# Kernel optimization log

Measured on AMD Instinct MI355X. Metric: run time of the kernel, lower is better.

Reference implementation:

```python
import jax, jax.numpy as jnp
import numpy as np

B, S, DIM, HEADS, MLP = 2, 2048, 1024, 16, 4096
DH = DIM // HEADS
LN_EPS = 1e-5


def layernorm(x, g, b):
    m = x.mean(-1, keepdims=True)
    v = ((x - m) ** 2).mean(-1, keepdims=True)
    return (x - m) / jnp.sqrt(v + LN_EPS) * g + b


def rope(x):
    # x: [B, H, S, dh]; interleaved-pair RoPE (rotary_embedding_torch convention)
    dh = x.shape[-1]
    s = x.shape[-2]
    inv_freq = 1.0 / (10000.0 ** (jnp.arange(0, dh, 2, dtype=jnp.float32) / dh))
    freqs = jnp.arange(s, dtype=jnp.float32)[:, None] * inv_freq[None, :]  # [S, dh/2]
    cos = jnp.repeat(jnp.cos(freqs), 2, axis=-1)  # [S, dh]
    sin = jnp.repeat(jnp.sin(freqs), 2, axis=-1)
    xp = x.reshape(x.shape[:-1] + (dh // 2, 2))
    x_rot = jnp.stack([-xp[..., 1], xp[..., 0]], axis=-1).reshape(x.shape)
    return x * cos + x_rot * sin


def setup_inputs() -> dict:
    key = jax.random.key(0)
    ks = jax.random.split(key, 10)
    w = 0.02
    return {
        "x": jax.random.normal(ks[0], (B, S, DIM), jnp.float32),
        "bias": jax.random.normal(ks[1], (B, S, S), jnp.float32) * 0.1,
        "ln1_g": jnp.ones((DIM,), jnp.float32),
        "ln1_b": jnp.zeros((DIM,), jnp.float32),
        "W_qkv": jax.random.normal(ks[2], (DIM, 3 * DIM), jnp.float32) * w,
        "W_o": jax.random.normal(ks[3], (DIM, DIM), jnp.float32) * w,
        "ln2_g": jnp.ones((DIM,), jnp.float32),
        "ln2_b": jnp.zeros((DIM,), jnp.float32),
        "W1": jax.random.normal(ks[4], (DIM, MLP), jnp.float32) * w,
        "b1": jnp.zeros((MLP,), jnp.float32),
        "W2": jax.random.normal(ks[5], (MLP, DIM), jnp.float32) * w,
        "b2": jnp.zeros((DIM,), jnp.float32),
        "pad_mask": jnp.zeros((B, S), jnp.int32),
    }


def reference(x, bias, ln1_g, ln1_b, W_qkv, W_o, ln2_g, ln2_b, W1, b1, W2, b2, pad_mask):
    b, s, d = x.shape
    h, dh = HEADS, DH
    res = x
    x1 = layernorm(x, ln1_g, ln1_b)
    qkv = (x1 @ W_qkv).reshape(b, s, h, 3 * dh)
    q, k, v = jnp.split(qkv, 3, axis=-1)            # each [B,S,H,dh]
    q = rope(q.transpose(0, 2, 1, 3))               # [B,H,S,dh]
    k = rope(k.transpose(0, 2, 1, 3))
    v = v.transpose(0, 2, 1, 3)
    scores = jnp.einsum("bhqd,bhkd->bhqk", q, k) * (dh ** -0.5)
    scores = scores + bias[:, None]                 # additive bias per batch
    key_mask = pad_mask.astype(bool)[:, None, None, :]
    scores = jnp.where(key_mask, -jnp.inf, scores)
    attn = jax.nn.softmax(scores, axis=-1)          # dropout = identity (eval)
    out = jnp.einsum("bhqk,bhkd->bhqd", attn, v)
    out = out.transpose(0, 2, 1, 3).reshape(b, s, d)
    x = res + out @ W_o
    res2 = x
    x2 = layernorm(x, ln2_g, ln2_b)
    mlp = jax.nn.gelu(x2 @ W1 + b1, approximate=False) @ W2 + b2
    return res2 + mlp
```

## Files before the change

### kernel.cpp

```cpp
#include <hip/hip_runtime.h>
#include <hip/hip_bf16.h>

#define B_   2
#define S_   2048
#define DIM_ 1024
#define H_   16
#define DH_  64
#define MLP_ 4096

typedef __bf16 bf16x8 __attribute__((ext_vector_type(8)));
typedef float  f32x4  __attribute__((ext_vector_type(4)));

__device__ __forceinline__ ushort f2bf(float f) {
    union { float f; unsigned u; } x; x.f = f;
    unsigned r = x.u + 0x7FFFu + ((x.u >> 16) & 1u);
    return (ushort)(r >> 16);
}
__device__ __forceinline__ float bf2f(ushort b) {
    union { unsigned u; float f; } x; x.u = ((unsigned)b) << 16;
    return x.f;
}

#define GLOAD_LDS16(gptr, lptr)                                                        \
    __builtin_amdgcn_global_load_lds(                                                  \
        (const __attribute__((address_space(1))) unsigned int*)(const void*)(gptr),    \
        (__attribute__((address_space(3))) unsigned int*)(void*)(lptr), 16, 0, 0)

#define MFMA_BF16(a, b, c) __builtin_amdgcn_mfma_f32_16x16x32_bf16((a), (b), (c), 0, 0, 0)

__global__ __launch_bounds__(256) void transpose_all(const float* __restrict__ Wqkv, ushort* __restrict__ Wqkvt,
                                                     const float* __restrict__ Wo,   ushort* __restrict__ Wot,
                                                     const float* __restrict__ W1,   ushort* __restrict__ W1t,
                                                     const float* __restrict__ W2,   ushort* __restrict__ W2t) {
    int id = blockIdx.x;
    const float* in; ushort* outp; int K, N, nx;
    if (id < 3072)      { in = Wqkv; outp = Wqkvt; K = 1024; N = 3072; nx = 96;  }
    else if (id < 4096) { id -= 3072; in = Wo; outp = Wot;  K = 1024; N = 1024; nx = 32;  }
    else if (id < 8192) { id -= 4096; in = W1; outp = W1t;  K = 1024; N = 4096; nx = 128; }
    else                { id -= 8192; in = W2; outp = W2t;  K = 4096; N = 1024; nx = 32;  }
    int n0 = (id % nx) * 32, k0 = (id / nx) * 32;
    __shared__ float t[32][33];
    int tx = threadIdx.x, ty = threadIdx.y;
#pragma unroll
    for (int r = 0; r < 32; r += 8)
        t[ty + r][tx] = in[(size_t)(k0 + ty + r) * N + n0 + tx];
    __syncthreads();
#pragma unroll
    for (int r = 0; r < 32; r += 8)
        outp[(size_t)(n0 + ty + r) * K + k0 + tx] = f2bf(t[tx][ty + r]);
}

__global__ __launch_bounds__(256) void ln_kernel(const float* __restrict__ in,
                                                 const float* __restrict__ g,
                                                 const float* __restrict__ beta,
                                                 ushort* __restrict__ out) {
    int row = blockIdx.x;
    float4 v = reinterpret_cast<const float4*>(in + (size_t)row * DIM_)[threadIdx.x];
    float s = v.x + v.y + v.z + v.w;
    float s2 = v.x * v.x + v.y * v.y + v.z * v.z + v.w * v.w;
#pragma unroll
    for (int m = 1; m < 64; m <<= 1) { s += __shfl_xor(s, m); s2 += __shfl_xor(s2, m); }
    __shared__ float red[8];
    int wid = threadIdx.x >> 6;
    if ((threadIdx.x & 63) == 0) { red[wid] = s; red[4 + wid] = s2; }
    __syncthreads();
    s  = red[0] + red[1] + red[2] + red[3];
    s2 = red[4] + red[5] + red[6] + red[7];
    float mean = s * (1.f / DIM_);
    float var  = s2 * (1.f / DIM_) - mean * mean;
    float inv  = rsqrtf(var + 1e-5f);
    float4 gg = reinterpret_cast<const float4*>(g)[threadIdx.x];
    float4 bb = reinterpret_cast<const float4*>(beta)[threadIdx.x];
    ushort4 o;
    o.x = f2bf((v.x - mean) * inv * gg.x + bb.x);
    o.y = f2bf((v.y - mean) * inv * gg.y + bb.y);
    o.z = f2bf((v.z - mean) * inv * gg.z + bb.z);
    o.w = f2bf((v.w - mean) * inv * gg.w + bb.w);
    reinterpret_cast<ushort4*>(out + (size_t)row * DIM_)[threadIdx.x] = o;
}

template <int RM, int RN, bool BIAS, bool GELU, bool RES, bool OBF16>
__global__ __launch_bounds__(256) void gemm_bt(const ushort* __restrict__ A,
                                               const ushort* __restrict__ Bt,
                                               void* __restrict__ Cout,
                                               const float* __restrict__ bias,
                                               const float* __restrict__ resid,
                                               int M, int N, int K) {
    constexpr int BM = RM * 64, BN = RN * 64;
    __shared__ __align__(16) ushort As[2][BM * 32];
    __shared__ __align__(16) ushort Bs[2][BN * 32];
    int tid = threadIdx.x;
    int wid = tid >> 6, lane = tid & 63;
    int lr = lane & 15, lg = lane >> 4;

    int nbx = gridDim.x;
    int nwg = nbx * gridDim.y;
    int bid = blockIdx.y * nbx + blockIdx.x;
    int swz = (bid & 7) * (nwg >> 3) + (bid >> 3);
    int row0 = (swz / nbx) * BM, col0 = (swz % nbx) * BN;

    int wm = (wid >> 1) * (RM * 32), wn = (wid & 1) * (RN * 32);
    int srow = tid >> 2, scol = (tid & 3) * 8;

    f32x4 acc[RM * 2][RN * 2] = {};

    const ushort* gA = A + (size_t)(row0 + srow) * K + scol;
    const ushort* gB = Bt + (size_t)(col0 + srow) * K + scol;

    auto stage = [&](int buf, int kt) {
#pragma unroll
        for (int r = 0; r < RM; r++)
            GLOAD_LDS16(gA + (size_t)r * 64 * K + kt, As[buf] + r * 2048 + wid * 512);
#pragma unroll
        for (int r = 0; r < RN; r++)
            GLOAD_LDS16(gB + (size_t)r * 64 * K + kt, Bs[buf] + r * 2048 + wid * 512);
    };

    int nk = K >> 5;
    stage(0, 0);
    __syncthreads();

    for (int t = 0; t < nk; t++) {
        int cur = t & 1;
        if (t + 1 < nk) stage(cur ^ 1, (t + 1) << 5);
        bf16x8 af[RM * 2], bfr[RN * 2];
#pragma unroll
        for (int m = 0; m < RM * 2; m++)
            af[m] = *reinterpret_cast<const bf16x8*>(As[cur] + (wm + m * 16 + lr) * 32 + lg * 8);
#pragma unroll
        for (int n = 0; n < RN * 2; n++)
            bfr[n] = *reinterpret_cast<const bf16x8*>(Bs[cur] + (wn + n * 16 + lr) * 32 + lg * 8);
#pragma unroll
        for (int m = 0; m < RM * 2; m++)
#pragma unroll
            for (int n = 0; n < RN * 2; n++)
                acc[m][n] = MFMA_BF16(af[m], bfr[n], acc[m][n]);
        __syncthreads();
    }

#pragma unroll
    for (int m = 0; m < RM * 2; m++) {
#pragma unroll
        for (int n = 0; n < RN * 2; n++) {
            int col = col0 + wn + n * 16 + lr;
#pragma unroll
            for (int i = 0; i < 4; i++) {
                int row = row0 + wm + m * 16 + lg * 4 + i;
                float v = acc[m][n][i];
                if (BIAS) v += bias[col];
                if (GELU) v = 0.5f * v * (1.f + erff(v * 0.70710678118f));
                if (RES)  v += resid[(size_t)row * N + col];
                if (OBF16) ((ushort*)Cout)[(size_t)row * N + col] = f2bf(v);
                else       ((float*)Cout)[(size_t)row * N + col] = v;
            }
        }
    }
}

__global__ __launch_bounds__(256) void gemm_qkv(const ushort* __restrict__ A,
                                                const ushort* __restrict__ Bt,
                                                const float2* __restrict__ tab,
                                                ushort* __restrict__ Qr,
                                                ushort* __restrict__ Kr,
                                                ushort* __restrict__ VT) {
    const int K = DIM_, N = 3 * DIM_;
    __shared__ __align__(16) ushort As[2][128 * 32];
    __shared__ __align__(16) ushort Bs[2][128 * 32];
    int tid = threadIdx.x;
    int wid = tid >> 6, lane = tid & 63;
    int lr = lane & 15, lg = lane >> 4;

    int nbx = gridDim.x;
    int nwg = nbx * gridDim.y;
    int bid = blockIdx.y * nbx + blockIdx.x;
    int swz = (bid & 7) * (nwg >> 3) + (bid >> 3);
    int row0 = (swz / nbx) * 128, col0 = (swz % nbx) * 128;

    int wm = (wid >> 1) * 64, wn = (wid & 1) * 64;
    int srow = tid >> 2, scol = (tid & 3) * 8;

    f32x4 acc[4][4] = {};

    const ushort* gA = A + (size_t)(row0 + srow) * K + scol;
    const ushort* gB = Bt + (size_t)(col0 + srow) * K + scol;

    auto stage = [&](int buf, int kt) {
#pragma unroll
        for (int r = 0; r < 2; r++)
            GLOAD_LDS16(gA + (size_t)r * 64 * K + kt, As[buf] + r * 2048 + wid * 512);
#pragma unroll
        for (int r = 0; r < 2; r++)
            GLOAD_LDS16(gB + (size_t)r * 64 * K + kt, Bs[buf] + r * 2048 + wid * 512);
    };

    int nk = K >> 5;
    stage(0, 0);
    __syncthreads();

    for (int t = 0; t < nk; t++) {
        int cur = t & 1;
        if (t + 1 < nk) stage(cur ^ 1, (t + 1) << 5);
        bf16x8 af[4], bfr[4];
#pragma unroll
        for (int m = 0; m < 4; m++)
            af[m] = *reinterpret_cast<const bf16x8*>(As[cur] + (wm + m * 16 + lr) * 32 + lg * 8);
#pragma unroll
        for (int n = 0; n < 4; n++)
            bfr[n] = *reinterpret_cast<const bf16x8*>(Bs[cur] + (wn + n * 16 + lr) * 32 + lg * 8);
#pragma unroll
        for (int m = 0; m < 4; m++)
#pragma unroll
            for (int n = 0; n < 4; n++)
                acc[m][n] = MFMA_BF16(af[m], bfr[n], acc[m][n]);
        __syncthreads();
    }

#pragma unroll
    for (int n = 0; n < 4; n++) {
        int colb = col0 + wn + n * 16;
        int h    = colb / 192;
        int off  = colb % 192;
        int typ  = off >> 6;
        int d    = (off & 63) + lr;
#pragma unroll
        for (int m = 0; m < 4; m++) {
            if (typ < 2) {
                ushort* qk = (typ == 0) ? Qr : Kr;
#pragma unroll
                for (int i = 0; i < 4; i++) {
                    int row = row0 + wm + m * 16 + lg * 4 + i;
                    int b = row >> 11, s = row & (S_ - 1);
                    float v  = acc[m][n][i];
                    float pv = __shfl_xor(v, 1);
                    float2 cs = tab[(s << 5) + (d >> 1)];
                    float r = v * cs.x + ((d & 1) ? pv : -pv) * cs.y;
                    qk[((size_t)(b * H_ + h) * S_ + s) * DH_ + d] = f2bf(r);
                }
            } else {
                int row = row0 + wm + m * 16 + lg * 4;
                int b = row >> 11, s = row & (S_ - 1);
                ushort4 o4;
                o4.x = f2bf(acc[m][n][0]);
                o4.y = f2bf(acc[m][n][1]);
                o4.z = f2bf(acc[m][n][2]);
                o4.w = f2bf(acc[m][n][3]);
                *reinterpret_cast<ushort4*>(
                    VT + ((size_t)(b * H_ + h) * DH_ + d) * S_ + s) = o4;
            }
        }
    }
}

__global__ __launch_bounds__(256) void rope_table(float2* __restrict__ tab) {
    int i = blockIdx.x * 256 + threadIdx.x;
    int s = i >> 5, p = i & 31;
    float invf = __expf(-((float)(2 * p) / 64.f) * logf(10000.f));
    float a = (float)s * invf;
    tab[i] = make_float2(cosf(a), sinf(a));
}

__global__ __launch_bounds__(256) void attn_kernel(const ushort* __restrict__ Q,
                                                   const ushort* __restrict__ Kr,
                                                   const ushort* __restrict__ VT,
                                                   const float* __restrict__ bias,
                                                   const int* __restrict__ pad,
                                                   ushort* __restrict__ Out) {
    int bx = blockIdx.x;
    int qt = bx & 31, h = (bx >> 5) & 15, b = bx >> 9;
    __shared__ __align__(16) ushort Ks[64 * 72];
    __shared__ __align__(16) ushort Vs[64 * 72];
    __shared__ __align__(16) ushort Ps[64 * 72];
    int tid = threadIdx.x, wid = tid >> 6, lane = tid & 63;
    int lr = lane & 15, lg = lane >> 4;
    int q0 = qt * 64;
    const ushort* Qb = Q + ((size_t)(b * H_ + h) * S_) * DH_;
    const ushort* Kb = Kr + ((size_t)(b * H_ + h) * S_) * DH_;
    const ushort* Vb = VT + ((size_t)(b * H_ + h) * DH_) * S_;
    const float*  bb = bias + (size_t)b * S_ * S_;
    const int*    pb = pad + b * S_;

    bf16x8 qf[2];
#pragma unroll
    for (int ks = 0; ks < 2; ks++)
        qf[ks] = *reinterpret_cast<const bf16x8*>(
            Qb + (size_t)(q0 + wid * 16 + lr) * DH_ + ks * 32 + lg * 8);

    float mrow[4], lrow[4];
#pragma unroll
    for (int i = 0; i < 4; i++) { mrow[i] = -3e38f; lrow[i] = 0.f; }
    f32x4 o[4] = {};

    int sr = tid >> 3, sc = (tid & 7) * 8;
    const float scale = 0.125f;

    for (int kv0 = 0; kv0 < S_; kv0 += 64) {
        __syncthreads();
#pragma unroll
        for (int cc = 0; cc < 2; cc++) {
            int r = cc * 32 + sr;
            *reinterpret_cast<bf16x8*>(Ks + r * 72 + sc) =
                *reinterpret_cast<const bf16x8*>(Kb + (size_t)(kv0 + r) * DH_ + sc);
            *reinterpret_cast<bf16x8*>(Vs + r * 72 + sc) =
                *reinterpret_cast<const bf16x8*>(Vb + (size_t)r * S_ + kv0 + sc);
        }
        __syncthreads();

        f32x4 sa[4] = {};
#pragma unroll
        for (int n = 0; n < 4; n++) {
            bf16x8 k0 = *reinterpret_cast<const bf16x8*>(Ks + (n * 16 + lr) * 72 + lg * 8);
            bf16x8 k1 = *reinterpret_cast<const bf16x8*>(Ks + (n * 16 + lr) * 72 + 32 + lg * 8);
            sa[n] = MFMA_BF16(qf[0], k0, sa[n]);
            sa[n] = MFMA_BF16(qf[1], k1, sa[n]);
        }

        int pm[4];
#pragma unroll
        for (int n = 0; n < 4; n++) pm[n] = pb[kv0 + n * 16 + lr];

#pragma unroll
        for (int i = 0; i < 4; i++) {
            const float* brow = bb + (size_t)(q0 + wid * 16 + lg * 4 + i) * S_ + kv0;
            float sv[4];
            float rmax = -3e38f;
#pragma unroll
            for (int n = 0; n < 4; n++) {
                float s = sa[n][i] * scale + brow[n * 16 + lr];
                if (pm[n]) s = -1e30f;
                sv[n] = s;
                rmax = fmaxf(rmax, s);
            }
#pragma unroll
            for (int msk = 1; msk < 16; msk <<= 1) rmax = fmaxf(rmax, __shfl_xor(rmax, msk));
            float mnew = fmaxf(mrow[i], rmax);
            float resc = __expf(mrow[i] - mnew);
            mrow[i] = mnew;
            float ls = 0.f;
            int prow = (i << 2) | lg;
#pragma unroll
            for (int n = 0; n < 4; n++) {
                float p = __expf(sv[n] - mnew);
                ls += p;
                Ps[(wid * 16 + prow) * 72 + n * 16 + lr] = f2bf(p);
            }
            lrow[i] = lrow[i] * resc + ls;
#pragma unroll
            for (int fn = 0; fn < 4; fn++) o[fn][i] *= resc;
        }

        int plr = ((lr & 3) << 2) | (lr >> 2);
        bf16x8 pf0 = *reinterpret_cast<const bf16x8*>(Ps + (wid * 16 + plr) * 72 + lg * 8);
        bf16x8 pf1 = *reinterpret_cast<const bf16x8*>(Ps + (wid * 16 + plr) * 72 + 32 + lg * 8);

#pragma unroll
        for (int fn = 0; fn < 4; fn++) {
            bf16x8 v0 = *reinterpret_cast<const bf16x8*>(Vs + (fn * 16 + lr) * 72 + lg * 8);
            bf16x8 v1 = *reinterpret_cast<const bf16x8*>(Vs + (fn * 16 + lr) * 72 + 32 + lg * 8);
            o[fn] = MFMA_BF16(pf0, v0, o[fn]);
            o[fn] = MFMA_BF16(pf1, v1, o[fn]);
        }
    }

#pragma unroll
    for (int i = 0; i < 4; i++)
#pragma unroll
        for (int msk = 1; msk < 16; msk <<= 1) lrow[i] += __shfl_xor(lrow[i], msk);

#pragma unroll
    for (int fn = 0; fn < 4; fn++)
#pragma unroll
        for (int i = 0; i < 4; i++) {
            int qrow = q0 + wid * 16 + lg * 4 + i;
            Out[(size_t)(b * S_ + qrow) * DIM_ + h * DH_ + fn * 16 + lr] =
                f2bf(o[fn][i] / lrow[i]);
        }
}

extern "C" void kernel_launch(void* const* d_in, const int* in_sizes, int n_in,
                              void* d_out, int out_size, void* d_ws, size_t ws_size,
                              hipStream_t stream) {
    const float* x    = (const float*)d_in[0];
    const float* bias = (const float*)d_in[1];
    const float* ln1g = (const float*)d_in[2];
    const float* ln1b = (const float*)d_in[3];
    const float* Wqkv = (const float*)d_in[4];
    const float* Wo   = (const float*)d_in[5];
    const float* ln2g = (const float*)d_in[6];
    const float* ln2b = (const float*)d_in[7];
    const float* W1   = (const float*)d_in[8];
    const float* b1   = (const float*)d_in[9];
    const float* W2   = (const float*)d_in[10];
    const float* b2   = (const float*)d_in[11];
    const int*   pad  = (const int*)d_in[12];
    float* out = (float*)d_out;

    char* ws = (char*)d_ws;
    size_t off = 0;
    auto alloc = [&](size_t bytes) {
        char* p = ws + off;
        off += (bytes + 255) & ~(size_t)255;
        return (void*)p;
    };
    ushort* x1    = (ushort*)alloc((size_t)4096 * 1024 * 2);
    ushort* Wqkvt = (ushort*)alloc((size_t)3072 * 1024 * 2);
    float2* tab   = (float2*)alloc((size_t)S_ * 32 * 8);
    ushort* Qr    = (ushort*)alloc((size_t)B_ * H_ * S_ * DH_ * 2);
    ushort* Kr2   = (ushort*)alloc((size_t)B_ * H_ * S_ * DH_ * 2);
    ushort* attnO = (ushort*)alloc((size_t)4096 * 1024 * 2);
    ushort* Wot   = (ushort*)alloc((size_t)1024 * 1024 * 2);
    float*  xmid  = (float*)alloc((size_t)4096 * 1024 * 4);
    ushort* x2    = (ushort*)alloc((size_t)4096 * 1024 * 2);
    ushort* W1t   = (ushort*)alloc((size_t)4096 * 1024 * 2);
    ushort* h1    = (ushort*)alloc((size_t)4096 * 4096 * 2);
    ushort* W2t   = (ushort*)alloc((size_t)1024 * 4096 * 2);
    ushort* VT    = h1;

    dim3 tb(32, 8);
    transpose_all<<<12288, tb, 0, stream>>>(Wqkv, Wqkvt, Wo, Wot, W1, W1t, W2, W2t);

    rope_table<<<(S_ * 32) / 256, 256, 0, stream>>>(tab);

    ln_kernel<<<4096, 256, 0, stream>>>(x, ln1g, ln1b, x1);

    gemm_qkv<<<dim3(24, 32), 256, 0, stream>>>(x1, Wqkvt, tab, Qr, Kr2, VT);

    attn_kernel<<<B_ * H_ * (S_ / 64), 256, 0, stream>>>(Qr, Kr2, VT, bias, pad, attnO);

    gemm_bt<1, 2, false, false, true, false><<<dim3(8, 64), 256, 0, stream>>>(
        attnO, Wot, xmid, nullptr, x, 4096, 1024, 1024);

    ln_kernel<<<4096, 256, 0, stream>>>(xmid, ln2g, ln2b, x2);

    gemm_bt<2, 2, true, true, false, true><<<dim3(32, 32), 256, 0, stream>>>(
        x2, W1t, h1, b1, nullptr, 4096, 4096, 1024);

    gemm_bt<1, 2, true, false, true, false><<<dim3(8, 64), 256, 0, stream>>>(
        h1, W2t, out, b2, xmid, 4096, 1024, 4096);
}
```

Measured before the change: 332.5 us.

## Use 512-thread 128x256 tiles for QKV and W1 GEMMs; use native bf16 convert

Adds 512-thread GEMM variants with a 128x256 output tile, eight waves each owning a 64x64 sub-tile, and switches the QKV projection and the first MLP GEMM to them. The wider tile increases A-tile reuse and halves the workgroup count, cutting global loads per FLOP. The cost is more LDS per block and fewer blocks to fill the CUs. The float-to-bf16 helper now uses the compiler's native conversion instead of manual rounding bit tricks.

Result: faster. 314.8 us (median of 2 runs) (-5.3%).

```diff
diff --git a/kernel.cpp b/kernel.cpp
--- a/kernel.cpp
+++ b/kernel.cpp
@@ -12,9 +12,8 @@
 typedef float  f32x4  __attribute__((ext_vector_type(4)));
 
 __device__ __forceinline__ ushort f2bf(float f) {
-    union { float f; unsigned u; } x; x.f = f;
-    unsigned r = x.u + 0x7FFFu + ((x.u >> 16) & 1u);
-    return (ushort)(r >> 16);
+    __bf16 h = (__bf16)f;
+    return __builtin_bit_cast(ushort, h);
 }
 __device__ __forceinline__ float bf2f(ushort b) {
     union { unsigned u; float f; } x; x.u = ((unsigned)b) << 16;
@@ -157,15 +156,15 @@
     }
 }
 
-__global__ __launch_bounds__(256) void gemm_qkv(const ushort* __restrict__ A,
-                                                const ushort* __restrict__ Bt,
-                                                const float2* __restrict__ tab,
-                                                ushort* __restrict__ Qr,
-                                                ushort* __restrict__ Kr,
-                                                ushort* __restrict__ VT) {
-    const int K = DIM_, N = 3 * DIM_;
+template <bool BIAS, bool GELU, bool RES, bool OBF16>
+__global__ __launch_bounds__(512) void gemm_bt512(const ushort* __restrict__ A,
+                                                  const ushort* __restrict__ Bt,
+                                                  void* __restrict__ Cout,
+                                                  const float* __restrict__ bias,
+                                                  const float* __restrict__ resid,
+                                                  int M, int N, int K) {
     __shared__ __align__(16) ushort As[2][128 * 32];
-    __shared__ __align__(16) ushort Bs[2][128 * 32];
+    __shared__ __align__(16) ushort Bs[2][256 * 32];
     int tid = threadIdx.x;
     int wid = tid >> 6, lane = tid & 63;
     int lr = lane & 15, lg = lane >> 4;
@@ -174,9 +173,9 @@
     int nwg = nbx * gridDim.y;
     int bid = blockIdx.y * nbx + blockIdx.x;
     int swz = (bid & 7) * (nwg >> 3) + (bid >> 3);
-    int row0 = (swz / nbx) * 128, col0 = (swz % nbx) * 128;
-
-    int wm = (wid >> 1) * 64, wn = (wid & 1) * 64;
+    int row0 = (swz / nbx) * 128, col0 = (swz % nbx) * 256;
+
+    int wm = (wid >> 2) * 64, wn = (wid & 3) * 64;
     int srow = tid >> 2, scol = (tid & 3) * 8;
 
     f32x4 acc[4][4] = {};
@@ -185,12 +184,83 @@
     const ushort* gB = Bt + (size_t)(col0 + srow) * K + scol;
 
     auto stage = [&](int buf, int kt) {
-#pragma unroll
-        for (int r = 0; r < 2; r++)
-            GLOAD_LDS16(gA + (size_t)r * 64 * K + kt, As[buf] + r * 2048 + wid * 512);
-#pragma unroll
-        for (int r = 0; r < 2; r++)
-            GLOAD_LDS16(gB + (size_t)r * 64 * K + kt, Bs[buf] + r * 2048 + wid * 512);
+        GLOAD_LDS16(gA + kt, As[buf] + wid * 512);
+        GLOAD_LDS16(gB + kt, Bs[buf] + wid * 512);
+        GLOAD_LDS16(gB + (size_t)128 * K + kt, Bs[buf] + 4096 + wid * 512);
+    };
+
+    int nk = K >> 5;
+    stage(0, 0);
+    __syncthreads();
+
+    for (int t = 0; t < nk; t++) {
+        int cur = t & 1;
+        if (t + 1 < nk) stage(cur ^ 1, (t + 1) << 5);
+        bf16x8 af[4], bfr[4];
+#pragma unroll
+        for (int m = 0; m < 4; m++)
+            af[m] = *reinterpret_cast<const bf16x8*>(As[cur] + (wm + m * 16 + lr) * 32 + lg * 8);
+#pragma unroll
+        for (int n = 0; n < 4; n++)
+            bfr[n] = *reinterpret_cast<const bf16x8*>(Bs[cur] + (wn + n * 16 + lr) * 32 + lg * 8);
+#pragma unroll
+        for (int m = 0; m < 4; m++)
+#pragma unroll
+            for (int n = 0; n < 4; n++)
+                acc[m][n] = MFMA_BF16(af[m], bfr[n], acc[m][n]);
+        __syncthreads();
+    }
+
+#pragma unroll
+    for (int m = 0; m < 4; m++) {
+#pragma unroll
+        for (int n = 0; n < 4; n++) {
+            int col = col0 + wn + n * 16 + lr;
+#pragma unroll
+            for (int i = 0; i < 4; i++) {
+                int row = row0 + wm + m * 16 + lg * 4 + i;
+                float v = acc[m][n][i];
+                if (BIAS) v += bias[col];
+                if (GELU) v = 0.5f * v * (1.f + erff(v * 0.70710678118f));
+                if (RES)  v += resid[(size_t)row * N + col];
+                if (OBF16) ((ushort*)Cout)[(size_t)row * N + col] = f2bf(v);
+                else       ((float*)Cout)[(size_t)row * N + col] = v;
+            }
+        }
+    }
+}
+
+__global__ __launch_bounds__(512) void gemm_qkv512(const ushort* __restrict__ A,
+                                                   const ushort* __restrict__ Bt,
+                                                   const float2* __restrict__ tab,
+                                                   ushort* __restrict__ Qr,
+                                                   ushort* __restrict__ Kr,
+                                                   ushort* __restrict__ VT) {
+    const int K = DIM_;
+    __shared__ __align__(16) ushort As[2][128 * 32];
+    __shared__ __align__(16) ushort Bs[2][256 * 32];
+    int tid = threadIdx.x;
+    int wid = tid >> 6, lane = tid & 63;
+    int lr = lane & 15, lg = lane >> 4;
+
+    int nbx = gridDim.x;
+    int nwg = nbx * gridDim.y;
+    int bid = blockIdx.y * nbx + blockIdx.x;
+    int swz = (bid & 7) * (nwg >> 3) + (bid >> 3);
+    int row0 = (swz / nbx) * 128, col0 = (swz % nbx) * 256;
+
+    int wm = (wid >> 2) * 64, wn = (wid & 3) * 64;
+    int srow = tid >> 2, scol = (tid & 3) * 8;
+
+    f32x4 acc[4][4] = {};
+
+    const ushort* gA = A + (size_t)(row0 + srow) * K + scol;
+    const ushort* gB = Bt + (size_t)(col0 + srow) * K + scol;
+
+    auto stage = [&](int buf, int kt) {
+        GLOAD_LDS16(gA + kt, As[buf] + wid * 512);
+        GLOAD_LDS16(gB + kt, Bs[buf] + wid * 512);
+        GLOAD_LDS16(gB + (size_t)128 * K + kt, Bs[buf] + 4096 + wid * 512);
     };
 
     int nk = K >> 5;
@@ -422,7 +492,7 @@
 
     ln_kernel<<<4096, 256, 0, stream>>>(x, ln1g, ln1b, x1);
 
-    gemm_qkv<<<dim3(24, 32), 256, 0, stream>>>(x1, Wqkvt, tab, Qr, Kr2, VT);
+    gemm_qkv512<<<dim3(12, 32), 512, 0, stream>>>(x1, Wqkvt, tab, Qr, Kr2, VT);
 
     attn_kernel<<<B_ * H_ * (S_ / 64), 256, 0, stream>>>(Qr, Kr2, VT, bias, pad, attnO);
 
@@ -431,7 +501,7 @@
 
     ln_kernel<<<4096, 256, 0, stream>>>(xmid, ln2g, ln2b, x2);
 
-    gemm_bt<2, 2, true, true, false, true><<<dim3(32, 32), 256, 0, stream>>>(
+    gemm_bt512<true, true, false, true><<<dim3(16, 32), 512, 0, stream>>>(
         x2, W1t, h1, b1, nullptr, 4096, 4096, 1024);
 
     gemm_bt<1, 2, true, false, true, false><<<dim3(8, 64), 256, 0, stream>>>(
```
